# Performance work log

Measured on AMD Instinct MI355X. Metric: run time of the kernel, lower is better.

## Reference

```python
import jax, jax.numpy as jnp
import numpy as np

C, H, W, N = 256, 256, 256, 512
ROI_SIZE = 7


def setup_inputs() -> dict:
    key = jax.random.key(0)
    k1, k2, k3 = jax.random.split(key, 3)
    feature = jax.random.normal(k1, (C, H, W), dtype=jnp.float32)
    # rois layout: (y1, x1, y2, x2), valid boxes inside the map
    start = jax.random.uniform(k2, (N, 2), jnp.float32, 0.0, H / 2)
    size = jax.random.uniform(k3, (N, 2), jnp.float32, 8.0, H / 2)
    rois = jnp.concatenate([start, start + size], axis=-1)
    return {"feature": feature, "rois": rois}


def _bilinear(feature, x, y):
    # feature: [C, H, W]; x, y: [...] float sample coords.
    # Faithful to the torch code: corners are clamped BEFORE computing the
    # interpolation weights (y - y1, y2 - y, etc.).
    h, w = feature.shape[-2:]
    y1 = jnp.floor(y).astype(jnp.int32)
    y2 = y1 + 1
    x1 = jnp.floor(x).astype(jnp.int32)
    x2 = x1 + 1
    y1 = jnp.clip(y1, 0, h - 1)
    y2 = jnp.clip(y2, 0, h - 1)
    x1 = jnp.clip(x1, 0, w - 1)
    x2 = jnp.clip(x2, 0, w - 1)
    wy1 = y - y1  # dist to top (clamped) corner
    wy2 = y2 - y
    wx1 = x - x1
    wx2 = x2 - x
    f11 = feature[:, y1, x1]  # [C, ...]
    f12 = feature[:, y1, x2]
    f21 = feature[:, y2, x1]
    f22 = feature[:, y2, x2]
    p = f11 * wx2 + f12 * wx1
    q = f21 * wx2 + f22 * wx1
    return p * wy2 + q * wy1


def reference(feature, rois):
    # feature: [C, H, W]; rois: [N, 4] = (y1, x1, y2, x2)
    R = ROI_SIZE
    n_roi = rois.shape[0]
    c = feature.shape[0]
    stride_h = (rois[:, 2] - rois[:, 0]) / R  # [N]
    stride_w = (rois[:, 3] - rois[:, 1]) / R  # [N]
    bins = jnp.arange(R, dtype=feature.dtype)
    y_base = rois[:, 0, None] + stride_h[:, None] * bins  # [N, 7]
    x_base = rois[:, 1, None] + stride_w[:, None] * bins  # [N, 7]
    # two sample points per bin, at 1/3 and 2/3 of the bin stride
    ys = jnp.stack([y_base + stride_h[:, None] / 3,
                    y_base + 2 * stride_h[:, None] / 3], axis=-1)  # [N, 7, 2]
    xs = jnp.stack([x_base + stride_w[:, None] / 3,
                    x_base + 2 * stride_w[:, None] / 3], axis=-1)  # [N, 7, 2]
    # all (y_sample, x_sample) combos per (roi, bin_m, bin_n): [N, 7, 7, 2, 2]
    Y = ys[:, :, None, :, None]
    X = xs[:, None, :, None, :]
    Yb, Xb = jnp.broadcast_arrays(Y, X)
    vals = _bilinear(feature, Xb, Yb)  # [C, N, 7, 7, 2, 2]
    # Faithful to torch.max(cat(...)) on a [C, 4] tensor: a GLOBAL max over
    # both channels and the 4 sample points, broadcast back to all channels.
    pooled = vals.max(axis=(0, -2, -1))  # [N, 7, 7]
    return jnp.broadcast_to(pooled[:, None, :, :], (n_roi, c, R, R))
```

## Files before the change

kernel.cpp:

```cpp
#include <hip/hip_runtime.h>

#define CCH 256
#define HH  256
#define WW  256
#define HWSZ (HH * WW)
#define NROI 512
#define RBIN 7
#define NBIN (RBIN * RBIN)
#define TFEAT_BYTES ((size_t)HWSZ * CCH * 2)
#define POOLED_BYTES ((size_t)NROI * NBIN * 4)

__device__ __forceinline__ unsigned short f2bf_rne(float f) {
    unsigned u = __float_as_uint(f);
    u = (u + 0x7fffu + ((u >> 16) & 1u)) >> 16;
    return (unsigned short)u;
}
__device__ __forceinline__ float bf2f(unsigned short h) {
    return __uint_as_float(((unsigned)h) << 16);
}

__global__ __launch_bounds__(256)
void transpose_chw_to_hwc_bf16(const float* __restrict__ feat,
                               unsigned short* __restrict__ tfeat)
{
    __shared__ float tile[32][33];
    const int tx = threadIdx.x;
    const int ty = threadIdx.y;
    const int hw0 = blockIdx.x * 32;
    const int c0  = blockIdx.y * 32;

    #pragma unroll
    for (int j = 0; j < 4; ++j) {
        const int c = c0 + ty + j * 8;
        tile[ty + j * 8][tx] = feat[(size_t)c * HWSZ + hw0 + tx];
    }
    __syncthreads();
    #pragma unroll
    for (int j = 0; j < 4; ++j) {
        const int hw = hw0 + ty + j * 8;
        const int c  = c0 + tx;
        tfeat[(size_t)hw * CCH + c] = f2bf_rne(tile[tx][ty + j * 8]);
    }
}

__global__ __launch_bounds__(256)
void roialign_sample_hwc(const unsigned short* __restrict__ tfeat,
                         const float* __restrict__ rois,
                         float* __restrict__ pooled)
{
    const int blk = blockIdx.x;
    const int n   = blk / NBIN;
    const int bin = blk % NBIN;
    const int by  = bin / RBIN;
    const int bx  = bin % RBIN;

    const int t    = threadIdx.x;
    const int wave = t >> 6;
    const int lane = t & 63;
    const int sy   = wave >> 1;
    const int sx   = wave & 1;

    const float y0  = rois[n * 4 + 0];
    const float x0  = rois[n * 4 + 1];
    const float sh  = (rois[n * 4 + 2] - y0) / (float)RBIN;
    const float sw  = (rois[n * 4 + 3] - x0) / (float)RBIN;

    const float y = y0 + sh * (float)by +
                    ((sy == 0) ? (sh / 3.0f) : (2.0f * sh / 3.0f));
    const float x = x0 + sw * (float)bx +
                    ((sx == 0) ? (sw / 3.0f) : (2.0f * sw / 3.0f));

    int iy1 = (int)floorf(y);
    int iy2 = iy1 + 1;
    int ix1 = (int)floorf(x);
    int ix2 = ix1 + 1;
    iy1 = min(max(iy1, 0), HH - 1);
    iy2 = min(max(iy2, 0), HH - 1);
    ix1 = min(max(ix1, 0), WW - 1);
    ix2 = min(max(ix2, 0), WW - 1);

    const float wy1 = y - (float)iy1;
    const float wy2 = (float)iy2 - y;
    const float wx1 = x - (float)ix1;
    const float wx2 = (float)ix2 - x;

    const ushort4* p11 = (const ushort4*)(tfeat + (size_t)(iy1 * WW + ix1) * CCH);
    const ushort4* p12 = (const ushort4*)(tfeat + (size_t)(iy1 * WW + ix2) * CCH);
    const ushort4* p21 = (const ushort4*)(tfeat + (size_t)(iy2 * WW + ix1) * CCH);
    const ushort4* p22 = (const ushort4*)(tfeat + (size_t)(iy2 * WW + ix2) * CCH);

    const ushort4 a = p11[lane];
    const ushort4 b = p12[lane];
    const ushort4 c = p21[lane];
    const ushort4 d = p22[lane];

    float m = -INFINITY;
    {
        float p, q, v;
        p = bf2f(a.x) * wx2 + bf2f(b.x) * wx1;
        q = bf2f(c.x) * wx2 + bf2f(d.x) * wx1;
        v = p * wy2 + q * wy1;  m = fmaxf(m, v);
        p = bf2f(a.y) * wx2 + bf2f(b.y) * wx1;
        q = bf2f(c.y) * wx2 + bf2f(d.y) * wx1;
        v = p * wy2 + q * wy1;  m = fmaxf(m, v);
        p = bf2f(a.z) * wx2 + bf2f(b.z) * wx1;
        q = bf2f(c.z) * wx2 + bf2f(d.z) * wx1;
        v = p * wy2 + q * wy1;  m = fmaxf(m, v);
        p = bf2f(a.w) * wx2 + bf2f(b.w) * wx1;
        q = bf2f(c.w) * wx2 + bf2f(d.w) * wx1;
        v = p * wy2 + q * wy1;  m = fmaxf(m, v);
    }

    #pragma unroll
    for (int off = 32; off > 0; off >>= 1)
        m = fmaxf(m, __shfl_xor(m, off, 64));

    __shared__ float wmax[4];
    if (lane == 0) wmax[wave] = m;
    __syncthreads();
    if (t == 0) {
        float r = fmaxf(fmaxf(wmax[0], wmax[1]), fmaxf(wmax[2], wmax[3]));
        pooled[n * NBIN + bin] = r;
    }
}

__global__ __launch_bounds__(256)
void roialign_broadcast(const float* __restrict__ pooled,
                        float* __restrict__ out)
{
    const int n = blockIdx.x;
    const int t = threadIdx.x;
    __shared__ float p[NBIN];
    if (t < NBIN) p[t] = pooled[n * NBIN + t];
    __syncthreads();
    float* o = out + (size_t)n * (CCH * NBIN);
    for (int idx = t; idx < CCH * NBIN; idx += 256)
        o[idx] = p[idx % NBIN];
}

__global__ __launch_bounds__(256)
void roialign_direct_kernel(const float* __restrict__ feat,
                            const float* __restrict__ rois,
                            float* __restrict__ out)
{
    const int n = blockIdx.x;
    const int t = threadIdx.x;
    __shared__ float ptmax[196];
    __shared__ float pooled[NBIN];

    const float y0  = rois[n * 4 + 0];
    const float x0  = rois[n * 4 + 1];
    const float sh  = (rois[n * 4 + 2] - y0) / (float)RBIN;
    const float sw  = (rois[n * 4 + 3] - x0) / (float)RBIN;

    const bool active = (t < 196);
    int off11 = 0, off12 = 0, off21 = 0, off22 = 0;
    float wx1 = 0.f, wx2 = 0.f, wy1 = 0.f, wy2 = 0.f;
    if (active) {
        const int py = t / 14, px = t % 14;
        const int by = py >> 1, sy = py & 1;
        const int bx = px >> 1, sx = px & 1;
        const float y = y0 + sh * (float)by + ((sy == 0) ? (sh / 3.0f) : (2.0f * sh / 3.0f));
        const float x = x0 + sw * (float)bx + ((sx == 0) ? (sw / 3.0f) : (2.0f * sw / 3.0f));
        int iy1 = (int)floorf(y), iy2 = iy1 + 1;
        int ix1 = (int)floorf(x), ix2 = ix1 + 1;
        iy1 = min(max(iy1, 0), HH - 1); iy2 = min(max(iy2, 0), HH - 1);
        ix1 = min(max(ix1, 0), WW - 1); ix2 = min(max(ix2, 0), WW - 1);
        wy1 = y - (float)iy1; wy2 = (float)iy2 - y;
        wx1 = x - (float)ix1; wx2 = (float)ix2 - x;
        off11 = iy1 * WW + ix1; off12 = iy1 * WW + ix2;
        off21 = iy2 * WW + ix1; off22 = iy2 * WW + ix2;
    }
    if (active) {
        float m = -INFINITY;
        const float* f = feat;
        #pragma unroll 4
        for (int c = 0; c < CCH; ++c) {
            const float p = f[off11] * wx2 + f[off12] * wx1;
            const float q = f[off21] * wx2 + f[off22] * wx1;
            m = fmaxf(m, p * wy2 + q * wy1);
            f += HWSZ;
        }
        ptmax[t] = m;
    }
    __syncthreads();
    if (t < NBIN) {
        const int by = t / RBIN, bx = t % RBIN;
        const int p00 = (2 * by) * 14 + 2 * bx;
        pooled[t] = fmaxf(fmaxf(ptmax[p00], ptmax[p00 + 1]),
                          fmaxf(ptmax[p00 + 14], ptmax[p00 + 15]));
    }
    __syncthreads();
    float* o = out + (size_t)n * (CCH * NBIN);
    for (int idx = t; idx < CCH * NBIN; idx += 256)
        o[idx] = pooled[idx % NBIN];
}

extern "C" void kernel_launch(void* const* d_in, const int* in_sizes, int n_in,
                              void* d_out, int out_size, void* d_ws, size_t ws_size,
                              hipStream_t stream)
{
    const float* feat = (const float*)d_in[0];
    const float* rois = (const float*)d_in[1];
    float* out = (float*)d_out;

    if (ws_size < TFEAT_BYTES + POOLED_BYTES) {
        roialign_direct_kernel<<<NROI, 256, 0, stream>>>(feat, rois, out);
        return;
    }

    unsigned short* tfeat = (unsigned short*)d_ws;
    float* pooled = (float*)((char*)d_ws + TFEAT_BYTES);

    dim3 tgrid(HWSZ / 32, CCH / 32);
    dim3 tblk(32, 8);
    transpose_chw_to_hwc_bf16<<<tgrid, tblk, 0, stream>>>(feat, tfeat);

    roialign_sample_hwc<<<NROI * NBIN, 256, 0, stream>>>(tfeat, rois, pooled);

    roialign_broadcast<<<NROI, 256, 0, stream>>>(pooled, out);
}
```

Baseline: 139.1 us.

## Fuse ROI sampling and broadcast into one kernel, widen transpose tiles

Merges the per-bin sampling kernel and the broadcast kernel into one 1024-thread block per ROI. Each wave handles several sample points, the partial maxima are reduced in shared memory, and the block writes the output with nontemporal stores. This removes one launch and the pooled round-trip through global memory. The transpose now handles 64 positions per block with float2 nontemporal loads and packed ushort2 stores. The trade-off is fewer blocks in the sampling stage (512 instead of about 25k), which lowers parallelism for the gather loads.

```diff
diff --git a/kernel.cpp b/kernel.cpp
--- a/kernel.cpp
+++ b/kernel.cpp
@@ -8,7 +8,8 @@
 #define RBIN 7
 #define NBIN (RBIN * RBIN)
 #define TFEAT_BYTES ((size_t)HWSZ * CCH * 2)
-#define POOLED_BYTES ((size_t)NROI * NBIN * 4)
+
+typedef float vfloat2 __attribute__((ext_vector_type(2)));
 
 __device__ __forceinline__ unsigned short f2bf_rne(float f) {
     unsigned u = __float_as_uint(f);
@@ -23,119 +24,122 @@
 void transpose_chw_to_hwc_bf16(const float* __restrict__ feat,
                                unsigned short* __restrict__ tfeat)
 {
-    __shared__ float tile[32][33];
-    const int tx = threadIdx.x;
-    const int ty = threadIdx.y;
-    const int hw0 = blockIdx.x * 32;
+    __shared__ float tile[32][65];
+    const int t   = threadIdx.x;
+    const int hw0 = blockIdx.x * 64;
     const int c0  = blockIdx.y * 32;
 
     #pragma unroll
     for (int j = 0; j < 4; ++j) {
-        const int c = c0 + ty + j * 8;
-        tile[ty + j * 8][tx] = feat[(size_t)c * HWSZ + hw0 + tx];
+        const int cl = (t >> 5) + j * 8;
+        const int hl = (t & 31) * 2;
+        const vfloat2 v = __builtin_nontemporal_load(
+            (const vfloat2*)(feat + (size_t)(c0 + cl) * HWSZ + hw0 + hl));
+        tile[cl][hl]     = v.x;
+        tile[cl][hl + 1] = v.y;
     }
     __syncthreads();
     #pragma unroll
     for (int j = 0; j < 4; ++j) {
-        const int hw = hw0 + ty + j * 8;
-        const int c  = c0 + tx;
-        tfeat[(size_t)hw * CCH + c] = f2bf_rne(tile[tx][ty + j * 8]);
-    }
-}
-
-__global__ __launch_bounds__(256)
-void roialign_sample_hwc(const unsigned short* __restrict__ tfeat,
-                         const float* __restrict__ rois,
-                         float* __restrict__ pooled)
-{
-    const int blk = blockIdx.x;
-    const int n   = blk / NBIN;
-    const int bin = blk % NBIN;
-    const int by  = bin / RBIN;
-    const int bx  = bin % RBIN;
-
+        const int hl = (t >> 4) + j * 16;
+        const int cl = (t & 15) * 2;
+        ushort2 w;
+        w.x = f2bf_rne(tile[cl][hl]);
+        w.y = f2bf_rne(tile[cl + 1][hl]);
+        *(ushort2*)(tfeat + (size_t)(hw0 + hl) * CCH + c0 + cl) = w;
+    }
+}
+
+__global__ __launch_bounds__(1024)
+void roialign_fused(const unsigned short* __restrict__ tfeat,
+                    const float* __restrict__ rois,
+                    float* __restrict__ out)
+{
+    const int n    = blockIdx.x;
     const int t    = threadIdx.x;
     const int wave = t >> 6;
     const int lane = t & 63;
-    const int sy   = wave >> 1;
-    const int sx   = wave & 1;
-
-    const float y0  = rois[n * 4 + 0];
-    const float x0  = rois[n * 4 + 1];
-    const float sh  = (rois[n * 4 + 2] - y0) / (float)RBIN;
-    const float sw  = (rois[n * 4 + 3] - x0) / (float)RBIN;
-
-    const float y = y0 + sh * (float)by +
-                    ((sy == 0) ? (sh / 3.0f) : (2.0f * sh / 3.0f));
-    const float x = x0 + sw * (float)bx +
-                    ((sx == 0) ? (sw / 3.0f) : (2.0f * sw / 3.0f));
-
-    int iy1 = (int)floorf(y);
-    int iy2 = iy1 + 1;
-    int ix1 = (int)floorf(x);
-    int ix2 = ix1 + 1;
-    iy1 = min(max(iy1, 0), HH - 1);
-    iy2 = min(max(iy2, 0), HH - 1);
-    ix1 = min(max(ix1, 0), WW - 1);
-    ix2 = min(max(ix2, 0), WW - 1);
-
-    const float wy1 = y - (float)iy1;
-    const float wy2 = (float)iy2 - y;
-    const float wx1 = x - (float)ix1;
-    const float wx2 = (float)ix2 - x;
-
-    const ushort4* p11 = (const ushort4*)(tfeat + (size_t)(iy1 * WW + ix1) * CCH);
-    const ushort4* p12 = (const ushort4*)(tfeat + (size_t)(iy1 * WW + ix2) * CCH);
-    const ushort4* p21 = (const ushort4*)(tfeat + (size_t)(iy2 * WW + ix1) * CCH);
-    const ushort4* p22 = (const ushort4*)(tfeat + (size_t)(iy2 * WW + ix2) * CCH);
-
-    const ushort4 a = p11[lane];
-    const ushort4 b = p12[lane];
-    const ushort4 c = p21[lane];
-    const ushort4 d = p22[lane];
-
-    float m = -INFINITY;
-    {
-        float p, q, v;
-        p = bf2f(a.x) * wx2 + bf2f(b.x) * wx1;
-        q = bf2f(c.x) * wx2 + bf2f(d.x) * wx1;
-        v = p * wy2 + q * wy1;  m = fmaxf(m, v);
-        p = bf2f(a.y) * wx2 + bf2f(b.y) * wx1;
-        q = bf2f(c.y) * wx2 + bf2f(d.y) * wx1;
-        v = p * wy2 + q * wy1;  m = fmaxf(m, v);
-        p = bf2f(a.z) * wx2 + bf2f(b.z) * wx1;
-        q = bf2f(c.z) * wx2 + bf2f(d.z) * wx1;
-        v = p * wy2 + q * wy1;  m = fmaxf(m, v);
-        p = bf2f(a.w) * wx2 + bf2f(b.w) * wx1;
-        q = bf2f(c.w) * wx2 + bf2f(d.w) * wx1;
-        v = p * wy2 + q * wy1;  m = fmaxf(m, v);
-    }
-
+
+    __shared__ float pmax[196];
+    __shared__ float pooled[NBIN];
+
+    const float y0 = rois[n * 4 + 0];
+    const float x0 = rois[n * 4 + 1];
+    const float sh = (rois[n * 4 + 2] - y0) / (float)RBIN;
+    const float sw = (rois[n * 4 + 3] - x0) / (float)RBIN;
+
+    for (int p = wave; p < 196; p += 16) {
+        const int py = p / 14;
+        const int px = p % 14;
+        const int by = py >> 1, sy = py & 1;
+        const int bx = px >> 1, sx = px & 1;
+
+        const float y = y0 + sh * (float)by +
+                        ((sy == 0) ? (sh / 3.0f) : (2.0f * sh / 3.0f));
+        const float x = x0 + sw * (float)bx +
+                        ((sx == 0) ? (sw / 3.0f) : (2.0f * sw / 3.0f));
+
+        int iy1 = (int)floorf(y);
+        int iy2 = iy1 + 1;
+        int ix1 = (int)floorf(x);
+        int ix2 = ix1 + 1;
+        iy1 = min(max(iy1, 0), HH - 1);
+        iy2 = min(max(iy2, 0), HH - 1);
+        ix1 = min(max(ix1, 0), WW - 1);
+        ix2 = min(max(ix2, 0), WW - 1);
+
+        const float wy1 = y - (float)iy1;
+        const float wy2 = (float)iy2 - y;
+        const float wx1 = x - (float)ix1;
+        const float wx2 = (float)ix2 - x;
+
+        const ushort4 a = ((const ushort4*)(tfeat + (size_t)(iy1 * WW + ix1) * CCH))[lane];
+        const ushort4 b = ((const ushort4*)(tfeat + (size_t)(iy1 * WW + ix2) * CCH))[lane];
+        const ushort4 c = ((const ushort4*)(tfeat + (size_t)(iy2 * WW + ix1) * CCH))[lane];
+        const ushort4 d = ((const ushort4*)(tfeat + (size_t)(iy2 * WW + ix2) * CCH))[lane];
+
+        float m;
+        {
+            float pp, qq, v0, v1;
+            pp = bf2f(a.x) * wx2 + bf2f(b.x) * wx1;
+            qq = bf2f(c.x) * wx2 + bf2f(d.x) * wx1;
+            v0 = pp * wy2 + qq * wy1;
+            pp = bf2f(a.y) * wx2 + bf2f(b.y) * wx1;
+            qq = bf2f(c.y) * wx2 + bf2f(d.y) * wx1;
+            v1 = pp * wy2 + qq * wy1;
+            m = fmaxf(v0, v1);
+            pp = bf2f(a.z) * wx2 + bf2f(b.z) * wx1;
+            qq = bf2f(c.z) * wx2 + bf2f(d.z) * wx1;
+            v0 = pp * wy2 + qq * wy1;
+            pp = bf2f(a.w) * wx2 + bf2f(b.w) * wx1;
+            qq = bf2f(c.w) * wx2 + bf2f(d.w) * wx1;
+            v1 = pp * wy2 + qq * wy1;
+            m = fmaxf(m, fmaxf(v0, v1));
+        }
+
+        #pragma unroll
+        for (int off = 32; off > 0; off >>= 1)
+            m = fmaxf(m, __shfl_xor(m, off, 64));
+
+        if (lane == 0) pmax[p] = m;
+    }
+    __syncthreads();
+
+    if (t < NBIN) {
+        const int by = t / RBIN, bx = t % RBIN;
+        const int p00 = (2 * by) * 14 + 2 * bx;
+        pooled[t] = fmaxf(fmaxf(pmax[p00],      pmax[p00 + 1]),
+                          fmaxf(pmax[p00 + 14], pmax[p00 + 15]));
+    }
+    __syncthreads();
+
+    float* o = out + (size_t)n * (CCH * NBIN);
     #pragma unroll
-    for (int off = 32; off > 0; off >>= 1)
-        m = fmaxf(m, __shfl_xor(m, off, 64));
-
-    __shared__ float wmax[4];
-    if (lane == 0) wmax[wave] = m;
-    __syncthreads();
-    if (t == 0) {
-        float r = fmaxf(fmaxf(wmax[0], wmax[1]), fmaxf(wmax[2], wmax[3]));
-        pooled[n * NBIN + bin] = r;
-    }
-}
-
-__global__ __launch_bounds__(256)
-void roialign_broadcast(const float* __restrict__ pooled,
-                        float* __restrict__ out)
-{
-    const int n = blockIdx.x;
-    const int t = threadIdx.x;
-    __shared__ float p[NBIN];
-    if (t < NBIN) p[t] = pooled[n * NBIN + t];
-    __syncthreads();
-    float* o = out + (size_t)n * (CCH * NBIN);
-    for (int idx = t; idx < CCH * NBIN; idx += 256)
-        o[idx] = p[idx % NBIN];
+    for (int k = 0; k < 13; ++k) {
+        const int idx = t + k * 1024;
+        if (idx < CCH * NBIN)
+            __builtin_nontemporal_store(pooled[idx % NBIN], o + idx);
+    }
 }
 
 __global__ __launch_bounds__(256)
@@ -204,19 +208,15 @@
     const float* rois = (const float*)d_in[1];
     float* out = (float*)d_out;
 
-    if (ws_size < TFEAT_BYTES + POOLED_BYTES) {
+    if (ws_size < TFEAT_BYTES) {
         roialign_direct_kernel<<<NROI, 256, 0, stream>>>(feat, rois, out);
         return;
     }
 
     unsigned short* tfeat = (unsigned short*)d_ws;
-    float* pooled = (float*)((char*)d_ws + TFEAT_BYTES);
-
-    dim3 tgrid(HWSZ / 32, CCH / 32);
-    dim3 tblk(32, 8);
-    transpose_chw_to_hwc_bf16<<<tgrid, tblk, 0, stream>>>(feat, tfeat);
-
-    roialign_sample_hwc<<<NROI * NBIN, 256, 0, stream>>>(tfeat, rois, pooled);
-
-    roialign_broadcast<<<NROI, 256, 0, stream>>>(pooled, out);
-}
+
+    dim3 tgrid(HWSZ / 64, CCH / 32);
+    transpose_chw_to_hwc_bf16<<<tgrid, 256, 0, stream>>>(feat, tfeat);
+
+    roialign_fused<<<NROI, 1024, 0, stream>>>(tfeat, rois, out);
+}
```

New measurement: 135.7 us. -2.5%, faster.
